# Kernel tuning notes

Measured on AMD Instinct MI355X. Metric: run time of the kernel, lower is better.

Reference implementation:

```python
import jax, jax.numpy as jnp
import numpy as np

SEQ = 2048
HID = 1024
NH = 16
HD = HID // NH


def setup_inputs() -> dict:
    key = jax.random.key(0)
    ks = jax.random.split(key, 5)
    s = 0.02
    return {
        "hidden_states": jax.random.normal(ks[0], (SEQ, HID), dtype=jnp.float32),
        "w_attn": jax.random.normal(ks[1], (HID, 3 * HID), dtype=jnp.float32) * s,
        "b_attn": jax.random.normal(ks[2], (3 * HID,), dtype=jnp.float32) * s,
        "w_proj": jax.random.normal(ks[3], (HID, HID), dtype=jnp.float32) * s,
        "b_proj": jax.random.normal(ks[4], (HID,), dtype=jnp.float32) * s,
    }


def reference(hidden_states, w_attn, b_attn, w_proj, b_proj):
    S = hidden_states.shape[0]
    qkv = hidden_states @ w_attn + b_attn          # [S, 3H]
    q, k, v = jnp.split(qkv, 3, axis=-1)
    q = q.reshape(S, NH, HD)
    k = k.reshape(S, NH, HD)
    v = v.reshape(S, NH, HD)
    sm_scale = 1.0 / np.sqrt(HD).astype(np.float32)
    # explicit scores [h, q, k] in fp32, as in the torch module
    scores = jnp.einsum('qhd,khd->hqk', q.astype(jnp.float32), k.astype(jnp.float32))
    scores = scores * sm_scale
    causal = jnp.tril(jnp.ones((S, S), dtype=bool))  # [q, k]
    scores = jnp.where(causal[None, :, :], scores, -jnp.inf)
    probs = jax.nn.softmax(scores, axis=-1)
    attn = jnp.einsum('hqk,khd->qhd', probs, v.astype(jnp.float32))  # [S, NH, HD]
    attn = attn.reshape(S, HID).astype(hidden_states.dtype)
    return attn @ w_proj + b_proj
```

## Files before the change

### kernel.cpp

```cpp
#include <hip/hip_runtime.h>
#include <cstdint>
#include <cstddef>

#define SEQ 2048
#define HID 1024
#define NHEAD 16
#define HDIM 64

typedef _Float16 f16;
typedef f16 half8 __attribute__((ext_vector_type(8)));
typedef f16 half4 __attribute__((ext_vector_type(4)));
typedef float f32x4 __attribute__((ext_vector_type(4)));

#define ASYNC_COPY16(g, l)                                                    \
  __builtin_amdgcn_global_load_lds(                                           \
      (const __attribute__((address_space(1))) void*)(const void*)(g),        \
      (__attribute__((address_space(3))) void*)(void*)(l), 16, 0, 0)

__global__ __launch_bounds__(256) void prologue(
    const float* __restrict__ h, const float* __restrict__ wa,
    const float* __restrict__ wp, f16* __restrict__ h16,
    f16* __restrict__ waT, f16* __restrict__ wpT) {
  const int b = blockIdx.x, tid = threadIdx.x;
  if (b >= 4096) {
    int i = ((b - 4096) * 256 + tid) * 4;
    float4 v = *(const float4*)(h + i);
    half4 o;
    o[0] = (f16)v.x; o[1] = (f16)v.y; o[2] = (f16)v.z; o[3] = (f16)v.w;
    *(half4*)(h16 + i) = o;
    return;
  }
  const float* src; f16* dst; int C, bx, by;
  if (b < 3072) { src = wa; dst = waT; C = 3072; bx = b % 96; by = b / 96; }
  else { int t = b - 3072; src = wp; dst = wpT; C = 1024; bx = t & 31; by = t >> 5; }
  __shared__ float tile[32][33];
  const int tx = tid & 31, ty = tid >> 5;
  const int c0 = bx * 32, r0 = by * 32;
#pragma unroll
  for (int i = 0; i < 32; i += 8)
    tile[ty + i][tx] = src[(size_t)(r0 + ty + i) * C + c0 + tx];
  __syncthreads();
#pragma unroll
  for (int i = 0; i < 32; i += 8)
    dst[(size_t)(c0 + ty + i) * 1024 + r0 + tx] = (f16)tile[tx][ty + i];
}

template <int BM, int BN, bool OUT16>
__global__ __launch_bounds__(256) void gemm_f16(
    const f16* __restrict__ A, const f16* __restrict__ Bt,
    const float* __restrict__ bias, void* __restrict__ Cout, int M, int N,
    int K) {
  constexpr int FM = BM / 32, FN = BN / 32;
  __shared__ __align__(16) f16 sA[2][BM * 32];
  __shared__ __align__(16) f16 sB[2][BN * 32];
  const int tid = threadIdx.x;
  const int wave = tid >> 6, lane = tid & 63;
  const int quad = lane >> 4, l16 = lane & 15;
  const int m0 = blockIdx.y * BM, n0 = blockIdx.x * BN;
  const int wm = (wave >> 1) * (BM / 2), wn = (wave & 1) * (BN / 2);
  const int rowA = lane >> 2, chunkA = lane & 3;

  f32x4 acc[FM][FN] = {};

  for (int k0 = 0; k0 < K; k0 += 64) {
#pragma unroll
    for (int tt = 0; tt < 2; tt++) {
#pragma unroll
      for (int r = wave; r < BM / 16; r += 4)
        ASYNC_COPY16(
            A + (size_t)(m0 + r * 16 + rowA) * K + k0 + tt * 32 + chunkA * 8,
            &sA[tt][r * 512]);
#pragma unroll
      for (int r = wave; r < BN / 16; r += 4)
        ASYNC_COPY16(
            Bt + (size_t)(n0 + r * 16 + rowA) * K + k0 + tt * 32 + chunkA * 8,
            &sB[tt][r * 512]);
    }
    __syncthreads();

#pragma unroll
    for (int tt = 0; tt < 2; tt++) {
      half8 af[FM], bf[FN];
#pragma unroll
      for (int i = 0; i < FM; i++)
        af[i] = *(const half8*)&sA[tt][(wm + i * 16 + l16) * 32 + quad * 8];
#pragma unroll
      for (int j = 0; j < FN; j++)
        bf[j] = *(const half8*)&sB[tt][(wn + j * 16 + l16) * 32 + quad * 8];
#pragma unroll
      for (int i = 0; i < FM; i++)
#pragma unroll
        for (int j = 0; j < FN; j++)
          acc[i][j] = __builtin_amdgcn_mfma_f32_16x16x32_f16(af[i], bf[j],
                                                             acc[i][j], 0, 0, 0);
    }
    __syncthreads();
  }

#pragma unroll
  for (int i = 0; i < FM; i++) {
    int row = m0 + wm + i * 16 + quad * 4;
#pragma unroll
    for (int j = 0; j < FN; j++) {
      int col = n0 + wn + j * 16 + l16;
      float bv = bias[col];
#pragma unroll
      for (int r = 0; r < 4; r++) {
        float v = acc[i][j][r] + bv;
        if (OUT16)
          ((f16*)Cout)[(size_t)(row + r) * N + col] = (f16)v;
        else
          ((float*)Cout)[(size_t)(row + r) * N + col] = v;
      }
    }
  }
}

#define LROW 72
__global__ __launch_bounds__(256, 3) void attn_split(
    const f16* __restrict__ qkv, f16* __restrict__ out,
    f16* __restrict__ Opart, float* __restrict__ ml) {
  const int b = blockIdx.x;
  const int h = b / 72;
  const int t = b % 72;
  int m, c, nc, base = 0;
  if (t < 2) { m = t; c = 0; nc = 1; }
  else {
    int s = t - 2, acc = 0;
    m = 2; c = 0; nc = 2;
    for (int mm = 2; mm <= 15; mm++) {
      int n = (2 * mm + 5) >> 2;
      if (s < acc + n) { m = mm; c = s - acc; nc = n; base = acc; break; }
      acc += n;
    }
  }
  const int q0 = m * 128;
  const int T = 2 * m + 2;
  const int kt0 = c * 4;
  const int kt1 = (kt0 + 4 < T) ? kt0 + 4 : T;
  const int maskFrom = 2 * m;

  __shared__ __align__(16) f16 sK[64 * LROW];
  __shared__ __align__(16) f16 sVt[64 * LROW];
  __shared__ __align__(16) f16 sP[4][32 * LROW];

  const int tid = threadIdx.x;
  const int wave = tid >> 6, lane = tid & 63;
  const int quad = lane >> 4, l16 = lane & 15;

  const f16 qs = (f16)0.18033688f;
  half8 qf[2][2];
#pragma unroll
  for (int g = 0; g < 2; g++) {
    const f16* qb = qkv + (size_t)(q0 + wave * 32 + g * 16 + l16) * 3072 +
                    h * HDIM + quad * 8;
    qf[g][0] = *(const half8*)qb;
    qf[g][1] = *(const half8*)(qb + 32);
#pragma unroll
    for (int j = 0; j < 8; j++) { qf[g][0][j] *= qs; qf[g][1][j] *= qs; }
  }

  const f16* kbase = qkv + HID + h * HDIM;
  const f16* vbase = qkv + 2 * HID + h * HDIM;
  const int ks_row = tid >> 3, ks_cc = tid & 7;
  const int vs_d = tid & 63, vs_g = tid >> 6;

  f32x4 o[2][4] = {};
  float m_i[2] = {-1e30f, -1e30f}, l_i[2] = {0.f, 0.f};
  half8 kreg[2], vreg[2];

  auto prefetch = [&](int kt) {
    const int k0 = kt * 64;
#pragma unroll
    for (int i = 0; i < 2; i++) {
      kreg[i] = *(const half8*)(kbase + (size_t)(k0 + ks_row + i * 32) * 3072 +
                                ks_cc * 8);
      half8 col;
#pragma unroll
      for (int j = 0; j < 8; j++)
        col[j] = vbase[(size_t)(k0 + (vs_g + i * 4) * 8 + j) * 3072 + vs_d];
      vreg[i] = col;
    }
  };

  prefetch(kt0);
  for (int kt = kt0; kt < kt1; kt++) {
    const int k0 = kt * 64;
#pragma unroll
    for (int i = 0; i < 2; i++) {
      *(half8*)&sK[(ks_row + i * 32) * LROW + ks_cc * 8] = kreg[i];
      *(half8*)&sVt[vs_d * LROW + (vs_g + i * 4) * 8] = vreg[i];
    }
    __syncthreads();
    if (kt + 1 < kt1) prefetch(kt + 1);

    f32x4 sacc[2][4] = {};
#pragma unroll
    for (int kb = 0; kb < 4; kb++) {
      half8 kf0 = *(const half8*)&sK[(kb * 16 + l16) * LROW + quad * 8];
      half8 kf1 = *(const half8*)&sK[(kb * 16 + l16) * LROW + 32 + quad * 8];
#pragma unroll
      for (int g = 0; g < 2; g++) {
        sacc[g][kb] = __builtin_amdgcn_mfma_f32_16x16x32_f16(kf0, qf[g][0],
                                                             sacc[g][kb], 0, 0, 0);
        sacc[g][kb] = __builtin_amdgcn_mfma_f32_16x16x32_f16(kf1, qf[g][1],
                                                             sacc[g][kb], 0, 0, 0);
      }
    }
    if (kt >= maskFrom) {
#pragma unroll
      for (int g = 0; g < 2; g++) {
        const int qg = q0 + wave * 32 + g * 16 + l16;
#pragma unroll
        for (int kb = 0; kb < 4; kb++) {
          int kg = k0 + kb * 16 + quad * 4;
#pragma unroll
          for (int r = 0; r < 4; r++)
            if (kg + r > qg) sacc[g][kb][r] = -1e30f;
        }
      }
    }
#pragma unroll
    for (int g = 0; g < 2; g++) {
      float mx = -1e30f;
#pragma unroll
      for (int kb = 0; kb < 4; kb++)
#pragma unroll
        for (int r = 0; r < 4; r++) mx = fmaxf(mx, sacc[g][kb][r]);
      mx = fmaxf(mx, __shfl_xor(mx, 16));
      mx = fmaxf(mx, __shfl_xor(mx, 32));
      const float mnew = fmaxf(m_i[g], mx);
      const float alpha = exp2f(m_i[g] - mnew);
      float rs = 0.f;
#pragma unroll
      for (int kb = 0; kb < 4; kb++)
#pragma unroll
        for (int r = 0; r < 4; r++) {
          float p = exp2f(sacc[g][kb][r] - mnew);
          sacc[g][kb][r] = p;
          rs += p;
        }
      rs += __shfl_xor(rs, 16);
      rs += __shfl_xor(rs, 32);
      l_i[g] = l_i[g] * alpha + rs;
      m_i[g] = mnew;
#pragma unroll
      for (int j = 0; j < 4; j++)
#pragma unroll
        for (int r = 0; r < 4; r++) o[g][j][r] *= alpha;
      f16* pw = &sP[wave][(g * 16 + l16) * LROW];
#pragma unroll
      for (int kb = 0; kb < 4; kb++) {
        half4 pv;
#pragma unroll
        for (int r = 0; r < 4; r++) pv[r] = (f16)sacc[g][kb][r];
        *(half4*)&pw[kb * 16 + quad * 4] = pv;
      }
    }
#pragma unroll
    for (int j = 0; j < 4; j++) {
      half8 vf0 = *(const half8*)&sVt[(j * 16 + l16) * LROW + quad * 8];
      half8 vf1 = *(const half8*)&sVt[(j * 16 + l16) * LROW + 32 + quad * 8];
#pragma unroll
      for (int g = 0; g < 2; g++) {
        half8 pf0 = *(const half8*)&sP[wave][(g * 16 + l16) * LROW + quad * 8];
        half8 pf1 =
            *(const half8*)&sP[wave][(g * 16 + l16) * LROW + 32 + quad * 8];
        o[g][j] = __builtin_amdgcn_mfma_f32_16x16x32_f16(vf0, pf0, o[g][j], 0, 0, 0);
        o[g][j] = __builtin_amdgcn_mfma_f32_16x16x32_f16(vf1, pf1, o[g][j], 0, 0, 0);
      }
    }
    __syncthreads();
  }

  if (nc == 1) {
#pragma unroll
    for (int g = 0; g < 2; g++) {
      const float inv = 1.f / l_i[g];
      f16* orow =
          out + (size_t)(q0 + wave * 32 + g * 16 + l16) * HID + h * HDIM;
#pragma unroll
      for (int j = 0; j < 4; j++) {
        half4 hv;
#pragma unroll
        for (int r = 0; r < 4; r++) hv[r] = (f16)(o[g][j][r] * inv);
        *(half4*)&orow[j * 16 + quad * 4] = hv;
      }
    }
  } else {
    const int slot = h * 70 + base + c;
#pragma unroll
    for (int g = 0; g < 2; g++) {
      const int qrow = wave * 32 + g * 16 + l16;
      f16* op = Opart + (size_t)slot * 8192 + qrow * 64;
#pragma unroll
      for (int j = 0; j < 4; j++) {
        half4 hv;
#pragma unroll
        for (int r = 0; r < 4; r++) hv[r] = (f16)o[g][j][r];
        *(half4*)&op[j * 16 + quad * 4] = hv;
      }
      if (quad == 0) {
        ml[slot * 256 + qrow] = m_i[g];
        ml[slot * 256 + 128 + qrow] = l_i[g];
      }
    }
  }
}

__global__ __launch_bounds__(256) void attn_combine(
    const f16* __restrict__ Opart, const float* __restrict__ ml,
    f16* __restrict__ out) {
  int idx = blockIdx.x * 256 + threadIdx.x;
  int d = idx & 63;
  int row = (idx >> 6) & 127;
  int rest = idx >> 13;
  int mi = rest % 14;
  int h = rest / 14;
  int m = 2 + mi;
  int nc = (2 * m + 5) >> 2;
  int base = 0;
  for (int j = 2; j < m; j++) base += (2 * j + 5) >> 2;
  int slot0 = h * 70 + base;

  float M = -1e30f;
  for (int cc = 0; cc < nc; cc++)
    M = fmaxf(M, ml[(slot0 + cc) * 256 + row]);
  float L = 0.f, acc = 0.f;
  for (int cc = 0; cc < nc; cc++) {
    float w = exp2f(ml[(slot0 + cc) * 256 + row] - M);
    L += w * ml[(slot0 + cc) * 256 + 128 + row];
    acc += w * (float)Opart[(size_t)(slot0 + cc) * 8192 + row * 64 + d];
  }
  out[(size_t)(m * 128 + row) * HID + h * HDIM + d] = (f16)(acc / L);
}

extern "C" void kernel_launch(void* const* d_in, const int* in_sizes, int n_in,
                              void* d_out, int out_size, void* d_ws,
                              size_t ws_size, hipStream_t stream) {
  const float* h = (const float*)d_in[0];
  const float* wa = (const float*)d_in[1];
  const float* ba = (const float*)d_in[2];
  const float* wp = (const float*)d_in[3];
  const float* bp = (const float*)d_in[4];
  float* out = (float*)d_out;

  char* ws = (char*)d_ws;
  f16* h16 = (f16*)(ws);
  f16* waT = (f16*)(ws + (4u << 20));
  f16* wpT = (f16*)(ws + (10u << 20));
  f16* qkv = (f16*)(ws + (12u << 20));
  f16* attn = (f16*)(ws + (24u << 20));
  f16* Opart = (f16*)(ws + (28u << 20));
  float* mlbuf = (float*)(ws + (28u << 20) + 18350080);

  prologue<<<6144, 256, 0, stream>>>(h, wa, wp, h16, waT, wpT);
  gemm_f16<128, 128, true><<<dim3(24, 16), 256, 0, stream>>>(
      h16, waT, ba, qkv, SEQ, 3 * HID, HID);
  attn_split<<<1152, 256, 0, stream>>>(qkv, attn, Opart, mlbuf);
  attn_combine<<<7168, 256, 0, stream>>>(Opart, mlbuf, attn);
  gemm_f16<64, 64, false><<<dim3(16, 32), 256, 0, stream>>>(
      attn, wpT, bp, out, SEQ, HID, HID);
}
```

Baseline: 162.9 us.

## Fuse split-KV combine into attention via last-block atomic counter; retile QKV GEMM

Removes the separate attn_combine launch. Each split block now increments a per-(head, query-tile) atomic counter, and the last block to finish merges the partial outputs using the stored m/l values. The counters are zeroed in the prologue kernel. The QKV projection GEMM also switches from 128x128 to 128x64 tiles, doubling the grid to improve CU occupancy. The cost is that the merge now runs serially in one block per tile, adding fence and atomic overhead and a tail imbalance.

```diff
diff --git a/kernel.cpp b/kernel.cpp
--- a/kernel.cpp
+++ b/kernel.cpp
@@ -20,8 +20,9 @@
 __global__ __launch_bounds__(256) void prologue(
     const float* __restrict__ h, const float* __restrict__ wa,
     const float* __restrict__ wp, f16* __restrict__ h16,
-    f16* __restrict__ waT, f16* __restrict__ wpT) {
+    f16* __restrict__ waT, f16* __restrict__ wpT, int* __restrict__ cnt) {
   const int b = blockIdx.x, tid = threadIdx.x;
+  if (b == 0 && tid < 224) cnt[tid] = 0;
   if (b >= 4096) {
     int i = ((b - 4096) * 256 + tid) * 4;
     float4 v = *(const float4*)(h + i);
@@ -119,7 +120,7 @@
 #define LROW 72
 __global__ __launch_bounds__(256, 3) void attn_split(
     const f16* __restrict__ qkv, f16* __restrict__ out,
-    f16* __restrict__ Opart, float* __restrict__ ml) {
+    f16* __restrict__ Opart, float* __restrict__ ml, int* __restrict__ cnt) {
   const int b = blockIdx.x;
   const int h = b / 72;
   const int t = b % 72;
@@ -143,6 +144,7 @@
   __shared__ __align__(16) f16 sK[64 * LROW];
   __shared__ __align__(16) f16 sVt[64 * LROW];
   __shared__ __align__(16) f16 sP[4][32 * LROW];
+  __shared__ int s_last;
 
   const int tid = threadIdx.x;
   const int wave = tid >> 6, lane = tid & 63;
@@ -287,52 +289,50 @@
         *(half4*)&orow[j * 16 + quad * 4] = hv;
       }
     }
-  } else {
-    const int slot = h * 70 + base + c;
-#pragma unroll
-    for (int g = 0; g < 2; g++) {
-      const int qrow = wave * 32 + g * 16 + l16;
-      f16* op = Opart + (size_t)slot * 8192 + qrow * 64;
-#pragma unroll
-      for (int j = 0; j < 4; j++) {
-        half4 hv;
-#pragma unroll
-        for (int r = 0; r < 4; r++) hv[r] = (f16)o[g][j][r];
-        *(half4*)&op[j * 16 + quad * 4] = hv;
-      }
-      if (quad == 0) {
-        ml[slot * 256 + qrow] = m_i[g];
-        ml[slot * 256 + 128 + qrow] = l_i[g];
-      }
-    }
-  }
-}
-
-__global__ __launch_bounds__(256) void attn_combine(
-    const f16* __restrict__ Opart, const float* __restrict__ ml,
-    f16* __restrict__ out) {
-  int idx = blockIdx.x * 256 + threadIdx.x;
-  int d = idx & 63;
-  int row = (idx >> 6) & 127;
-  int rest = idx >> 13;
-  int mi = rest % 14;
-  int h = rest / 14;
-  int m = 2 + mi;
-  int nc = (2 * m + 5) >> 2;
-  int base = 0;
-  for (int j = 2; j < m; j++) base += (2 * j + 5) >> 2;
-  int slot0 = h * 70 + base;
-
-  float M = -1e30f;
-  for (int cc = 0; cc < nc; cc++)
-    M = fmaxf(M, ml[(slot0 + cc) * 256 + row]);
-  float L = 0.f, acc = 0.f;
-  for (int cc = 0; cc < nc; cc++) {
-    float w = exp2f(ml[(slot0 + cc) * 256 + row] - M);
-    L += w * ml[(slot0 + cc) * 256 + 128 + row];
-    acc += w * (float)Opart[(size_t)(slot0 + cc) * 8192 + row * 64 + d];
-  }
-  out[(size_t)(m * 128 + row) * HID + h * HDIM + d] = (f16)(acc / L);
+    return;
+  }
+
+  const int slot = h * 70 + base + c;
+#pragma unroll
+  for (int g = 0; g < 2; g++) {
+    const int qrow = wave * 32 + g * 16 + l16;
+    f16* op = Opart + (size_t)slot * 8192 + qrow * 64;
+#pragma unroll
+    for (int j = 0; j < 4; j++) {
+      half4 hv;
+#pragma unroll
+      for (int r = 0; r < 4; r++) hv[r] = (f16)o[g][j][r];
+      *(half4*)&op[j * 16 + quad * 4] = hv;
+    }
+    if (quad == 0) {
+      ml[slot * 256 + qrow] = m_i[g];
+      ml[slot * 256 + 128 + qrow] = l_i[g];
+    }
+  }
+
+  __syncthreads();
+  if (tid == 0) {
+    __threadfence();
+    s_last = (atomicAdd(&cnt[h * 14 + (m - 2)], 1) == nc - 1);
+  }
+  __syncthreads();
+  if (!s_last) return;
+  __threadfence();
+
+  const int slot0 = h * 70 + base;
+  for (int u = tid; u < 8192; u += 256) {
+    int row = u >> 6, d = u & 63;
+    float M = -1e30f;
+    for (int cc = 0; cc < nc; cc++)
+      M = fmaxf(M, ml[(slot0 + cc) * 256 + row]);
+    float L = 0.f, acc = 0.f;
+    for (int cc = 0; cc < nc; cc++) {
+      float w = exp2f(ml[(slot0 + cc) * 256 + row] - M);
+      L += w * ml[(slot0 + cc) * 256 + 128 + row];
+      acc += w * (float)Opart[(size_t)(slot0 + cc) * 8192 + row * 64 + d];
+    }
+    out[(size_t)(m * 128 + row) * HID + h * HDIM + d] = (f16)(acc / L);
+  }
 }
 
 extern "C" void kernel_launch(void* const* d_in, const int* in_sizes, int n_in,
@@ -353,12 +353,12 @@
   f16* attn = (f16*)(ws + (24u << 20));
   f16* Opart = (f16*)(ws + (28u << 20));
   float* mlbuf = (float*)(ws + (28u << 20) + 18350080);
-
-  prologue<<<6144, 256, 0, stream>>>(h, wa, wp, h16, waT, wpT);
-  gemm_f16<128, 128, true><<<dim3(24, 16), 256, 0, stream>>>(
+  int* cnt = (int*)(ws + (28u << 20) + 18350080 + 1146880);
+
+  prologue<<<6144, 256, 0, stream>>>(h, wa, wp, h16, waT, wpT, cnt);
+  gemm_f16<128, 64, true><<<dim3(48, 16), 256, 0, stream>>>(
       h16, waT, ba, qkv, SEQ, 3 * HID, HID);
-  attn_split<<<1152, 256, 0, stream>>>(qkv, attn, Opart, mlbuf);
-  attn_combine<<<7168, 256, 0, stream>>>(Opart, mlbuf, attn);
+  attn_split<<<1152, 256, 0, stream>>>(qkv, attn, Opart, mlbuf, cnt);
   gemm_f16<64, 64, false><<<dim3(16, 32), 256, 0, stream>>>(
       attn, wpT, bp, out, SEQ, HID, HID);
 }
```

Measured after the change: 451.7 us. 2.77x slower.
